# Optimization experiments

Hardware: AMD Instinct MI355X
Metric: run time of the kernel (lower is better)

The kernel has to match this reference:

```python
import jax, jax.numpy as jnp
import numpy as np

B, S, D, H = 2, 2048, 1024, 16
HD = D // H

def setup_inputs() -> dict:
    key = jax.random.key(0)
    ks = jax.random.split(key, 9)
    s = 1.0 / np.sqrt(D)
    inp = {"x": jax.random.normal(ks[0], (B, S, D), dtype=jnp.float32)}
    for i, name in enumerate(["q", "k", "v", "g"]):
        inp[f"W{name}"] = jax.random.uniform(ks[1 + i], (D, D), minval=-s, maxval=s, dtype=jnp.float32)
        inp[f"b{name}"] = jax.random.uniform(ks[5 + i], (D,), minval=-s, maxval=s, dtype=jnp.float32)
    return inp

def reference(x, Wq, bq, Wk, bk, Wv, bv, Wg, bg):
    # projections: [B,S,D] -> [B,H,S,HD]
    def proj(W, b):
        y = x @ W.T + b
        return y.reshape(B, S, H, HD).transpose(0, 2, 1, 3)
    q = proj(Wq, bq)
    k = proj(Wk, bk)
    v = proj(Wv, bv)
    g = proj(Wg, bg)
    qg = jax.nn.gelu(q * g, approximate=False)  # gate + activation before scores
    att = jnp.einsum("bhqd,bhkd->bhqk", qg, k)  # note: no 1/sqrt(d) scaling in original
    att = jax.nn.softmax(att, axis=-1)
    out = jnp.einsum("bhqk,bhkd->bhqd", att, v)
    return out.transpose(0, 2, 1, 3).reshape(B, S, D)
```

## Files before the change

### kernel.cpp

```cpp
#include <hip/hip_runtime.h>
#include <hip/hip_bf16.h>
#include <stdint.h>

#define PB 2
#define PS 2048
#define PD 1024
#define PH 16
#define PHD 64
#define PM (PB*PS)

typedef _Float16 half8 __attribute__((ext_vector_type(8)));
typedef _Float16 half4v __attribute__((ext_vector_type(4)));
typedef __fp16   fp16x2 __attribute__((ext_vector_type(2)));
typedef float    f32x4 __attribute__((ext_vector_type(4)));

__device__ __forceinline__ void ld_g2l_16(const void* g, void* l) {
  __builtin_amdgcn_global_load_lds(
      (const __attribute__((address_space(1))) unsigned int*)g,
      (__attribute__((address_space(3))) unsigned int*)l, 16, 0, 0);
}

__global__ void convert_all(const float* __restrict__ x,
                            const float* __restrict__ w0, const float* __restrict__ w1,
                            const float* __restrict__ w2, const float* __restrict__ w3,
                            _Float16* __restrict__ xh, _Float16* __restrict__ wh) {
  int i = blockIdx.x * blockDim.x + threadIdx.x;
  const float* src;
  _Float16* dst;
  int idx;
  if (blockIdx.y == 0) {
    src = x; dst = xh; idx = i;
  } else {
    int wsel = i >> 17;
    idx = i & 131071;
    src = (wsel==0)?w0:(wsel==1)?w1:(wsel==2)?w2:w3;
    dst = wh + (size_t)wsel * 1048576;
  }
  float4 f0 = reinterpret_cast<const float4*>(src)[2*idx];
  float4 f1 = reinterpret_cast<const float4*>(src)[2*idx+1];
  half8 o;
  o[0]=(_Float16)f0.x; o[1]=(_Float16)f0.y; o[2]=(_Float16)f0.z; o[3]=(_Float16)f0.w;
  o[4]=(_Float16)f1.x; o[5]=(_Float16)f1.y; o[6]=(_Float16)f1.z; o[7]=(_Float16)f1.w;
  reinterpret_cast<half8*>(dst)[idx] = o;
}

__global__ __launch_bounds__(256, 3) void proj_gemm(
    const _Float16* __restrict__ xh, const _Float16* __restrict__ wh,
    const float* __restrict__ bqp, const float* __restrict__ bgp,
    const float* __restrict__ bkp, const float* __restrict__ bvp,
    _Float16* __restrict__ qf, _Float16* __restrict__ gf,
    _Float16* __restrict__ kf, _Float16* __restrict__ vT)
{
  const int K = 1024;
  __shared__ _Float16 Sm[16384];
  const int z = blockIdx.z;
  const int wslot = (z==0)?0:(z==1)?3:(z==2)?1:2;
  const size_t woff = (size_t)wslot * (1024*1024);
  const float* bias = (z==0)?bqp:(z==1)?bgp:(z==2)?bkp:bvp;
  _Float16* outp = (z==0)?qf:(z==1)?gf:kf;
  const int m0 = blockIdx.x * 128;
  const int n0 = blockIdx.y * 128;
  const int t = threadIdx.x;
  const int lane = t & 63;
  const int w = t >> 6;
  const int wr = w >> 1, wc = w & 1;
  const int lm = lane & 15, quad = lane >> 4;
  const int scb = (((lane&3) ^ ((lane>>3)&3)))*8;
  const int rblk = ((quad ^ ((lm>>1)&3)))*8;

  auto stage = [&](int buf, int k0) {
    #pragma unroll
    for (int c=0;c<2;c++) {
      int lin = c*256 + t;
      int row = lin >> 2;
      size_t ga = (size_t)(m0+row)*K + k0 + scb;
      size_t gb = (size_t)(n0+row)*K + k0 + scb;
      int lo8 = (c*256 + w*64)*8;
      ld_g2l_16(&xh[ga],        &Sm[buf*4096 + lo8]);
      ld_g2l_16(&wh[woff + gb], &Sm[8192 + buf*4096 + lo8]);
    }
  };

  f32x4 acc[4][4];
  #pragma unroll
  for (int i=0;i<4;i++)
    #pragma unroll
    for (int j=0;j<4;j++) acc[i][j] = (f32x4){0.f,0.f,0.f,0.f};

  stage(0, 0);
  __syncthreads();

  for (int k0 = 0; k0 < K; k0 += 32) {
    const int cur = (k0 >> 5) & 1;
    if (k0 + 32 < K) stage(cur ^ 1, k0 + 32);

    half8 ah[4];
    #pragma unroll
    for (int i=0;i<4;i++)
      ah[i] = *reinterpret_cast<const half8*>(&Sm[cur*4096 + (wr*64 + i*16 + lm)*32 + rblk]);
    #pragma unroll
    for (int j=0;j<4;j++) {
      half8 b = *reinterpret_cast<const half8*>(&Sm[8192 + cur*4096 + (wc*64 + j*16 + lm)*32 + rblk]);
      #pragma unroll
      for (int i=0;i<4;i++)
        acc[i][j] = __builtin_amdgcn_mfma_f32_16x16x32_f16(ah[i], b, acc[i][j], 0,0,0);
    }
    __syncthreads();
  }

  if (z < 3) {
    #pragma unroll
    for (int j=0;j<4;j++) {
      int n = n0 + wc*64 + j*16 + lm;
      float bn = bias[n];
      #pragma unroll
      for (int i=0;i<4;i++) {
        int mb = m0 + wr*64 + i*16 + quad*4;
        #pragma unroll
        for (int r=0;r<4;r++)
          outp[(size_t)(mb+r)*PD + n] = (_Float16)(acc[i][j][r] + bn);
      }
    }
  } else {
    #pragma unroll
    for (int j=0;j<4;j++) {
      int nl = wc*64 + j*16 + lm;
      float bn = bias[n0 + nl];
      #pragma unroll
      for (int i=0;i<4;i++) {
        int tb = wr*64 + i*16 + quad*4;
        half4v pv;
        #pragma unroll
        for (int r=0;r<4;r++) pv[r] = (_Float16)(acc[i][j][r] + bn);
        int sw = (tb >> 3) ^ (nl & 15);
        *reinterpret_cast<half4v*>(&Sm[nl*128 + sw*8 + (tb & 7)]) = pv;
      }
    }
    __syncthreads();
    const int nl2 = t >> 1, co = (t & 1) * 8;
    const int hh = (n0 + nl2) >> 6, dd = (n0 + nl2) & 63;
    const int bb2 = m0 >> 11;
    const size_t vbase = ((size_t)((bb2*16 + hh)*64 + dd))*2048 + (m0 & 2047);
    #pragma unroll
    for (int c=0;c<8;c++) {
      int cc = co + c;
      half8 vv = *reinterpret_cast<const half8*>(&Sm[nl2*128 + ((cc ^ (nl2&15))<<3)]);
      *reinterpret_cast<half8*>(&vT[vbase + cc*8]) = vv;
    }
  }
}

__global__ __launch_bounds__(512) void flash_attn(
    const _Float16* __restrict__ Qf,
    const _Float16* __restrict__ Gf,
    const _Float16* __restrict__ Kp,
    const _Float16* __restrict__ VT,
    float* __restrict__ out)
{
  __shared__ _Float16 Ks[2][64*64];
  __shared__ _Float16 Vts[2][64*64];
  __shared__ _Float16 Pss[8][16*72];
  const int t = threadIdx.x;
  const int lane = t & 63, w = t >> 6;
  const int lm = lane & 15, quad = lane >> 4;
  const int hw = blockIdx.x + gridDim.x * blockIdx.y;
  const int logical = (hw & 7) * 64 + (hw >> 3);
  const int qblk = logical & 15;
  const int bh = logical >> 4;
  const int b = bh >> 4, h = bh & 15;
  const int qb = qblk * 128 + w * 16;
  const size_t kbase = (size_t)b * PS * PD + (size_t)h * PHD;
  const size_t vtb = (size_t)bh * 64 * 2048;

  const int lrow = lane >> 3;
  const int lcb  = ((lane & 7) ^ lrow) * 8;
  const int kblk0 = ((quad     ^ (lm&7)))*8;
  const int kblk1 = (((quad+4) ^ (lm&7)))*8;

  half8 qgf[2];
  {
    size_t qrow = kbase + (size_t)(qb + lm) * PD;
    half8 q0 = *reinterpret_cast<const half8*>(&Qf[qrow + quad*8]);
    half8 q1 = *reinterpret_cast<const half8*>(&Qf[qrow + 32 + quad*8]);
    half8 g0 = *reinterpret_cast<const half8*>(&Gf[qrow + quad*8]);
    half8 g1 = *reinterpret_cast<const half8*>(&Gf[qrow + 32 + quad*8]);
    #pragma unroll
    for (int e=0;e<8;e++) {
      float x0 = (float)q0[e] * (float)g0[e];
      float x1 = (float)q1[e] * (float)g1[e];
      float y0 = 0.5f * x0 * (1.0f + erff(x0 * 0.70710678118f));
      float y1 = 0.5f * x1 * (1.0f + erff(x1 * 0.70710678118f));
      qgf[0][e] = (_Float16)(y0 * 1.44269504f);
      qgf[1][e] = (_Float16)(y1 * 1.44269504f);
    }
  }

  half8 ones;
  #pragma unroll
  for (int e=0;e<8;e++) ones[e] = (_Float16)1.0f;

  f32x4 o[4];
  #pragma unroll
  for (int dc=0;dc<4;dc++) o[dc] = (f32x4){0.f,0.f,0.f,0.f};
  f32x4 o4 = (f32x4){0.f,0.f,0.f,0.f};

  const _Float16* kgp = &Kp[kbase + (size_t)(w*8 + lrow)*PD + lcb];
  const _Float16* vgp = &VT[vtb + (size_t)(w*8 + lrow)*2048 + lcb];

  const f32x4 sinit = {-11.54156036f, -11.54156036f, -11.54156036f, -11.54156036f};

  ld_g2l_16(kgp, &Ks[0][(w*8)*64]);
  ld_g2l_16(vgp, &Vts[0][(w*8)*64]);
  __syncthreads();

  for (int kt = 0; kt < PS; kt += 64) {
    const int buf = (kt >> 6) & 1;
    const bool nx = (kt + 64) < PS;
    if (nx) {
      ld_g2l_16(kgp + (size_t)(kt+64)*PD, &Ks[buf^1][(w*8)*64]);
      ld_g2l_16(vgp + kt + 64,            &Vts[buf^1][(w*8)*64]);
    }

    f32x4 s[4];
    __builtin_amdgcn_s_setprio(1);
    #pragma unroll
    for (int ns=0; ns<4; ns++) {
      const int rb = (ns*16 + lm)*64;
      half8 kf0 = *reinterpret_cast<const half8*>(&Ks[buf][rb + kblk0]);
      half8 kf1 = *reinterpret_cast<const half8*>(&Ks[buf][rb + kblk1]);
      f32x4 a = sinit;
      a = __builtin_amdgcn_mfma_f32_16x16x32_f16(kf0, qgf[0], a, 0,0,0);
      a = __builtin_amdgcn_mfma_f32_16x16x32_f16(kf1, qgf[1], a, 0,0,0);
      s[ns] = a;
    }
    __builtin_amdgcn_s_setprio(0);

    #pragma unroll
    for (int ns=0; ns<4; ns++) {
      float p0 = fminf(__builtin_amdgcn_exp2f(s[ns][0]), 60000.0f);
      float p1 = fminf(__builtin_amdgcn_exp2f(s[ns][1]), 60000.0f);
      float p2 = fminf(__builtin_amdgcn_exp2f(s[ns][2]), 60000.0f);
      float p3 = fminf(__builtin_amdgcn_exp2f(s[ns][3]), 60000.0f);
      union { struct { fp16x2 a, b; } s2; half4v v; } u;
      u.s2.a = __builtin_amdgcn_cvt_pkrtz(p0, p1);
      u.s2.b = __builtin_amdgcn_cvt_pkrtz(p2, p3);
      *reinterpret_cast<half4v*>(&Pss[w][lm*72 + ns*16 + quad*4]) = u.v;
    }

    half8 pa0 = *reinterpret_cast<const half8*>(&Pss[w][lm*72 + quad*8]);
    half8 pa1 = *reinterpret_cast<const half8*>(&Pss[w][lm*72 + 32 + quad*8]);
    __builtin_amdgcn_s_setprio(1);
    #pragma unroll
    for (int dc=0;dc<4;dc++) {
      const int vb = (dc*16 + lm)*64;
      half8 vb0 = *reinterpret_cast<const half8*>(&Vts[buf][vb + kblk0]);
      half8 vb1 = *reinterpret_cast<const half8*>(&Vts[buf][vb + kblk1]);
      o[dc] = __builtin_amdgcn_mfma_f32_16x16x32_f16(pa0, vb0, o[dc], 0,0,0);
      o[dc] = __builtin_amdgcn_mfma_f32_16x16x32_f16(pa1, vb1, o[dc], 0,0,0);
    }
    o4 = __builtin_amdgcn_mfma_f32_16x16x32_f16(pa0, ones, o4, 0,0,0);
    o4 = __builtin_amdgcn_mfma_f32_16x16x32_f16(pa1, ones, o4, 0,0,0);
    __builtin_amdgcn_s_setprio(0);

    __syncthreads();
  }

  #pragma unroll
  for (int r=0;r<4;r++) {
    float invr = 1.0f / o4[r];
    int row = qb + quad*4 + r;
    size_t ob = kbase + (size_t)row * PD;
    #pragma unroll
    for (int dc=0;dc<4;dc++) {
      out[ob + dc*16 + lm] = o[dc][r] * invr;
    }
  }
}

extern "C" void kernel_launch(void* const* d_in, const int* in_sizes, int n_in,
                              void* d_out, int out_size, void* d_ws, size_t ws_size,
                              hipStream_t stream) {
  const float* x  = (const float*)d_in[0];
  const float* Wq = (const float*)d_in[1];
  const float* bq = (const float*)d_in[2];
  const float* Wk = (const float*)d_in[3];
  const float* bk = (const float*)d_in[4];
  const float* Wv = (const float*)d_in[5];
  const float* bv = (const float*)d_in[6];
  const float* Wg = (const float*)d_in[7];
  const float* bg = (const float*)d_in[8];
  float* out = (float*)d_out;

  char* ws = (char*)d_ws;
  const size_t MB = 1u << 20;
  _Float16* xh = (_Float16*)(ws + 0*MB);
  _Float16* wh = (_Float16*)(ws + 8*MB);
  _Float16* qf = (_Float16*)(ws + 16*MB);
  _Float16* gf = (_Float16*)(ws + 24*MB);
  _Float16* kf = (_Float16*)(ws + 32*MB);
  _Float16* vT = (_Float16*)(ws + 40*MB);

  convert_all<<<dim3(2048, 2), 256, 0, stream>>>(x, Wq, Wk, Wv, Wg, xh, wh);

  proj_gemm<<<dim3(PM/128, PD/128, 4), 256, 0, stream>>>(
      xh, wh, bq, bg, bk, bv, qf, gf, kf, vT);

  flash_attn<<<dim3(PS/128, PB*PH), 512, 0, stream>>>(qf, gf, kf, vT, out);
}
```

Baseline: 182.4 us.

## Software-pipeline attention loop: overlap next tile's QK and exp with current PV

Restructures the flash attention K-loop so each iteration issues the QK^T MFMAs for tile t+1, then the PV MFMAs for tile t, then the exp and P conversion for tile t+1. K and V prefetch now runs two tiles ahead, with a third V shared-memory buffer so V for tile t stays resident while tile t+2 loads. The aim is to hide exp/VALU latency and LDS traffic behind matrix-core work from the other stage. It costs 8 KB more LDS and more live registers for the scores, which may lower occupancy.

New measurement: 181.5 us, median of 2. About the same (-0.5%).

```diff
diff --git a/kernel.cpp b/kernel.cpp
--- a/kernel.cpp
+++ b/kernel.cpp
@@ -158,7 +158,7 @@
     float* __restrict__ out)
 {
   __shared__ _Float16 Ks[2][64*64];
-  __shared__ _Float16 Vts[2][64*64];
+  __shared__ _Float16 Vts[3][64*64];
   __shared__ _Float16 Pss[8][16*72];
   const int t = threadIdx.x;
   const int lane = t & 63, w = t >> 6;
@@ -209,32 +209,27 @@
 
   const f32x4 sinit = {-11.54156036f, -11.54156036f, -11.54156036f, -11.54156036f};
 
-  ld_g2l_16(kgp, &Ks[0][(w*8)*64]);
-  ld_g2l_16(vgp, &Vts[0][(w*8)*64]);
+  ld_g2l_16(kgp,                   &Ks[0][(w*8)*64]);
+  ld_g2l_16(vgp,                   &Vts[0][(w*8)*64]);
+  ld_g2l_16(kgp + (size_t)64*PD,   &Ks[1][(w*8)*64]);
+  ld_g2l_16(vgp + 64,              &Vts[1][(w*8)*64]);
   __syncthreads();
 
-  for (int kt = 0; kt < PS; kt += 64) {
-    const int buf = (kt >> 6) & 1;
-    const bool nx = (kt + 64) < PS;
-    if (nx) {
-      ld_g2l_16(kgp + (size_t)(kt+64)*PD, &Ks[buf^1][(w*8)*64]);
-      ld_g2l_16(vgp + kt + 64,            &Vts[buf^1][(w*8)*64]);
-    }
-
+  half8 pa0, pa1;
+  {
     f32x4 s[4];
     __builtin_amdgcn_s_setprio(1);
     #pragma unroll
     for (int ns=0; ns<4; ns++) {
       const int rb = (ns*16 + lm)*64;
-      half8 kf0 = *reinterpret_cast<const half8*>(&Ks[buf][rb + kblk0]);
-      half8 kf1 = *reinterpret_cast<const half8*>(&Ks[buf][rb + kblk1]);
+      half8 kf0 = *reinterpret_cast<const half8*>(&Ks[0][rb + kblk0]);
+      half8 kf1 = *reinterpret_cast<const half8*>(&Ks[0][rb + kblk1]);
       f32x4 a = sinit;
       a = __builtin_amdgcn_mfma_f32_16x16x32_f16(kf0, qgf[0], a, 0,0,0);
       a = __builtin_amdgcn_mfma_f32_16x16x32_f16(kf1, qgf[1], a, 0,0,0);
       s[ns] = a;
     }
     __builtin_amdgcn_s_setprio(0);
-
     #pragma unroll
     for (int ns=0; ns<4; ns++) {
       float p0 = fminf(__builtin_amdgcn_exp2f(s[ns][0]), 60000.0f);
@@ -246,21 +241,63 @@
       u.s2.b = __builtin_amdgcn_cvt_pkrtz(p2, p3);
       *reinterpret_cast<half4v*>(&Pss[w][lm*72 + ns*16 + quad*4]) = u.v;
     }
-
-    half8 pa0 = *reinterpret_cast<const half8*>(&Pss[w][lm*72 + quad*8]);
-    half8 pa1 = *reinterpret_cast<const half8*>(&Pss[w][lm*72 + 32 + quad*8]);
+    pa0 = *reinterpret_cast<const half8*>(&Pss[w][lm*72 + quad*8]);
+    pa1 = *reinterpret_cast<const half8*>(&Pss[w][lm*72 + 32 + quad*8]);
+  }
+  __syncthreads();
+
+  for (int tt = 0; tt < 32; ++tt) {
+    const bool nx1 = (tt + 1) < 32;
+    const bool nx2 = (tt + 2) < 32;
+    if (nx2) {
+      ld_g2l_16(kgp + (size_t)(tt+2)*64*PD, &Ks[tt & 1][(w*8)*64]);
+      ld_g2l_16(vgp + (tt+2)*64,            &Vts[(tt+2)%3][(w*8)*64]);
+    }
+
+    f32x4 s[4];
+    if (nx1) {
+      __builtin_amdgcn_s_setprio(1);
+      #pragma unroll
+      for (int ns=0; ns<4; ns++) {
+        const int rb = (ns*16 + lm)*64;
+        half8 kf0 = *reinterpret_cast<const half8*>(&Ks[(tt+1)&1][rb + kblk0]);
+        half8 kf1 = *reinterpret_cast<const half8*>(&Ks[(tt+1)&1][rb + kblk1]);
+        f32x4 a = sinit;
+        a = __builtin_amdgcn_mfma_f32_16x16x32_f16(kf0, qgf[0], a, 0,0,0);
+        a = __builtin_amdgcn_mfma_f32_16x16x32_f16(kf1, qgf[1], a, 0,0,0);
+        s[ns] = a;
+      }
+      __builtin_amdgcn_s_setprio(0);
+    }
+
     __builtin_amdgcn_s_setprio(1);
     #pragma unroll
     for (int dc=0;dc<4;dc++) {
       const int vb = (dc*16 + lm)*64;
-      half8 vb0 = *reinterpret_cast<const half8*>(&Vts[buf][vb + kblk0]);
-      half8 vb1 = *reinterpret_cast<const half8*>(&Vts[buf][vb + kblk1]);
+      half8 vb0 = *reinterpret_cast<const half8*>(&Vts[tt%3][vb + kblk0]);
+      half8 vb1 = *reinterpret_cast<const half8*>(&Vts[tt%3][vb + kblk1]);
       o[dc] = __builtin_amdgcn_mfma_f32_16x16x32_f16(pa0, vb0, o[dc], 0,0,0);
       o[dc] = __builtin_amdgcn_mfma_f32_16x16x32_f16(pa1, vb1, o[dc], 0,0,0);
     }
     o4 = __builtin_amdgcn_mfma_f32_16x16x32_f16(pa0, ones, o4, 0,0,0);
     o4 = __builtin_amdgcn_mfma_f32_16x16x32_f16(pa1, ones, o4, 0,0,0);
     __builtin_amdgcn_s_setprio(0);
+
+    if (nx1) {
+      #pragma unroll
+      for (int ns=0; ns<4; ns++) {
+        float p0 = fminf(__builtin_amdgcn_exp2f(s[ns][0]), 60000.0f);
+        float p1 = fminf(__builtin_amdgcn_exp2f(s[ns][1]), 60000.0f);
+        float p2 = fminf(__builtin_amdgcn_exp2f(s[ns][2]), 60000.0f);
+        float p3 = fminf(__builtin_amdgcn_exp2f(s[ns][3]), 60000.0f);
+        union { struct { fp16x2 a, b; } s2; half4v v; } u;
+        u.s2.a = __builtin_amdgcn_cvt_pkrtz(p0, p1);
+        u.s2.b = __builtin_amdgcn_cvt_pkrtz(p2, p3);
+        *reinterpret_cast<half4v*>(&Pss[w][lm*72 + ns*16 + quad*4]) = u.v;
+      }
+      pa0 = *reinterpret_cast<const half8*>(&Pss[w][lm*72 + quad*8]);
+      pa1 = *reinterpret_cast<const half8*>(&Pss[w][lm*72 + 32 + quad*8]);
+    }
 
     __syncthreads();
   }
```
